# Performance work log

Hardware: AMD Instinct MI355X
Metric: run time of the kernel (lower is better)

Reference implementation:

```python
import math
import jax, jax.numpy as jnp
import numpy as np

H = 4
C_HID = 32

def setup_inputs() -> dict:
    key = jax.random.key(0)
    ks = jax.random.split(key, 8)
    B, N, C = 1, 256, 128
    q_x = jax.random.normal(ks[0], (B, N, N, C), dtype=jnp.float32)
    kv_x = jax.random.normal(ks[1], (B, N, N, C), dtype=jnp.float32)
    tri_bias = jax.random.normal(ks[2], (B, 1, H, N, N), dtype=jnp.float32)
    mask_bias = jnp.zeros((B, N, 1, 1, N), dtype=jnp.float32)
    mask = jnp.ones((B, N, N, N), dtype=jnp.float32)
    s = 1.0 / math.sqrt(C)
    Wq = jax.random.normal(ks[3], (C, H * C_HID), dtype=jnp.float32) * s
    Wk = jax.random.normal(ks[4], (C, H * C_HID), dtype=jnp.float32) * s
    Wv = jax.random.normal(ks[5], (C, H * C_HID), dtype=jnp.float32) * s
    Wg = jax.random.normal(ks[6], (C, H * C_HID), dtype=jnp.float32) * s
    Wo = jax.random.normal(ks[7], (H * C_HID, C), dtype=jnp.float32) * s
    return {"q_x": q_x, "kv_x": kv_x, "tri_bias": tri_bias, "mask_bias": mask_bias,
            "mask": mask, "Wq": Wq, "Wk": Wk, "Wv": Wv, "Wg": Wg, "Wo": Wo}

def reference(q_x, kv_x, tri_bias, mask_bias, mask, Wq, Wk, Wv, Wg, Wo):
    # q_x/kv_x: [B, N, Q, C]; mask is unused in the non-kernel path (mask_bias carries it)
    lead = q_x.shape[:-1]  # [B, N, Q]
    def split_heads(t):  # [..., H*C_HID] -> [..., H, L, C_HID]
        t = t.reshape(t.shape[:-1] + (H, C_HID))
        return jnp.swapaxes(t, -2, -3)
    q = split_heads(q_x @ Wq) / math.sqrt(C_HID)   # [B, N, H, Q, C_hid]
    k = split_heads(kv_x @ Wk)                      # [B, N, H, K, C_hid]
    v = split_heads(kv_x @ Wv)                      # [B, N, H, K, C_hid]
    a = jnp.einsum('bnhqc,bnhkc->bnhqk', q, k)
    a = a + mask_bias + tri_bias                    # biases broadcast over [B, N, H, Q, K]
    a = jax.nn.softmax(a, axis=-1)
    o = jnp.einsum('bnhqk,bnhkc->bnhqc', a, v)      # [B, N, H, Q, C_hid]
    o = jnp.swapaxes(o, -2, -3)                     # [B, N, Q, H, C_hid]
    g = jax.nn.sigmoid(q_x @ Wg).reshape(lead + (H, C_HID))
    o = o * g
    o = o.reshape(lead + (H * C_HID,))
    return o @ Wo                                   # [B, N, Q, C]
```

## Files before the change

kernel.cpp:

```cpp
#include <hip/hip_runtime.h>
#include <hip/hip_bf16.h>

#define NDIM 256
#define QDIM 256
#define CDIM 128
#define HH 4
#define DD 32
#define RROWS (NDIM * QDIM)

__device__ __forceinline__ float bf2f(unsigned short u) {
    unsigned int x = ((unsigned int)u) << 16;
    return __uint_as_float(x);
}
__device__ __forceinline__ unsigned short f2bf(float f) {
    unsigned int x = __float_as_uint(f);
    unsigned int lsb = (x >> 16) & 1u;
    x += 0x7fffu + lsb;
    return (unsigned short)(x >> 16);
}

typedef __bf16 bf16x8v __attribute__((ext_vector_type(8)));
typedef float  f32x4v  __attribute__((ext_vector_type(4)));
union frag_u { uint4 u; bf16x8v v; };

__device__ __forceinline__ bf16x8v cvt8(float4 f0, float4 f1) {
    bf16x8v r;
    r[0] = (__bf16)f0.x; r[1] = (__bf16)f0.y; r[2] = (__bf16)f0.z; r[3] = (__bf16)f0.w;
    r[4] = (__bf16)f1.x; r[5] = (__bf16)f1.y; r[6] = (__bf16)f1.z; r[7] = (__bf16)f1.w;
    return r;
}

__global__ __launch_bounds__(256, 1) void prep_weights(
    const float* __restrict__ Wq, const float* __restrict__ Wk,
    const float* __restrict__ Wv, const float* __restrict__ Wg,
    const float* __restrict__ Wo, unsigned short* __restrict__ wt)
{
    __shared__ unsigned short t[16][130];
    const int p  = blockIdx.x >> 3;
    const int ch = blockIdx.x & 7;
    const float* __restrict__ W = (p == 0) ? Wq : (p == 1) ? Wk :
                                  (p == 2) ? Wv : (p == 3) ? Wg : Wo;
    const int tid = threadIdx.x;
    for (int idx = tid; idx < 2048; idx += 256) {
        int k = idx >> 7, n = idx & 127;
        t[k][n] = f2bf(W[(ch * 16 + k) * 128 + n]);
    }
    __syncthreads();
    unsigned short* dst = wt + (size_t)p * 16384;
    for (int idx = tid; idx < 2048; idx += 256) {
        int n = idx >> 4, k = idx & 15;
        dst[n * 128 + ch * 16 + k] = t[k][n];
    }
}

__global__ __launch_bounds__(512, 4) void proj_mfma(
    const float* __restrict__ qx, const float* __restrict__ kvx,
    const unsigned short* __restrict__ wt,
    unsigned short* __restrict__ q_ws, unsigned short* __restrict__ k_ws,
    unsigned short* __restrict__ v_ws, unsigned short* __restrict__ g_ws)
{
    __shared__ unsigned short wl[2 * 16384];
    const int tid = threadIdx.x;
    const int pp = blockIdx.y;
    const float* __restrict__ X = pp ? kvx : qx;
    const unsigned short* __restrict__ WtA = wt + (size_t)(pp ? 1 : 0) * 16384;
    const unsigned short* __restrict__ WtB = wt + (size_t)(pp ? 2 : 3) * 16384;

    const int wv   = tid >> 6;
    const int lane = tid & 63;
    const int col  = lane & 15;
    const int quad = lane >> 4;
    const int r0   = blockIdx.x * 128 + wv * 16;

    const float* __restrict__ arow = X + (size_t)(r0 + col) * 128 + quad * 8;
    float4 f[4][2];
#pragma unroll
    for (int kt = 0; kt < 4; ++kt) {
        f[kt][0] = *(const float4*)(arow + kt * 32);
        f[kt][1] = *(const float4*)(arow + kt * 32 + 4);
    }

#pragma unroll
    for (int i = 0; i < 8; ++i) {
        int v = i * 512 + tid;
        int mat = v >> 11;
        int r = (v >> 4) & 127;
        int s = v & 15;
        const unsigned short* src = (mat ? WtB : WtA) + r * 128 + s * 8;
        uint4 d = *(const uint4*)src;
        *(uint4*)&wl[mat * 16384 + r * 128 + ((s ^ (r & 7)) << 3)] = d;
    }
    __syncthreads();

    frag_u a[4];
#pragma unroll
    for (int kt = 0; kt < 4; ++kt) a[kt].v = cvt8(f[kt][0], f[kt][1]);

    f32x4v accA[8], accB[8];
#pragma unroll
    for (int nt = 0; nt < 8; ++nt) {
        accA[nt] = (f32x4v){0.f, 0.f, 0.f, 0.f};
        accB[nt] = (f32x4v){0.f, 0.f, 0.f, 0.f};
    }

    const int x7 = col & 7;
#pragma unroll
    for (int kt = 0; kt < 4; ++kt) {
#pragma unroll
        for (int nt = 0; nt < 8; ++nt) {
            int off = nt * 2048 + col * 128 + ((((kt << 2) | quad) ^ x7) << 3);
            frag_u b0, b1;
            b0.u = *(const uint4*)&wl[off];
            b1.u = *(const uint4*)&wl[16384 + off];
            accA[nt] = __builtin_amdgcn_mfma_f32_16x16x32_bf16(a[kt].v, b0.v, accA[nt], 0, 0, 0);
            accB[nt] = __builtin_amdgcn_mfma_f32_16x16x32_bf16(a[kt].v, b1.v, accB[nt], 0, 0, 0);
        }
    }

#pragma unroll
    for (int r = 0; r < 4; ++r) {
        int row = r0 + quad * 4 + r;
        int n = row >> 8;
        int si = row & 255;
#pragma unroll
        for (int nt = 0; nt < 8; ++nt) {
            int c = nt * 16 + col;
            int h = c >> 5, d = c & 31;
            if (pp == 0) {
                float qv = accA[nt][r] * 0.17677669529663687f;
                q_ws[((size_t)(n * HH + h) * QDIM + si) * DD + d] = f2bf(qv);
                float s = 1.0f / (1.0f + __expf(-accB[nt][r]));
                g_ws[(size_t)row * 128 + c] = f2bf(s);
            } else {
                k_ws[((size_t)(n * HH + h) * QDIM + si) * DD + d] = f2bf(accA[nt][r]);
                v_ws[((size_t)(n * HH + h) * QDIM + si) * DD + d] = f2bf(accB[nt][r]);
            }
        }
    }
}

__global__ __launch_bounds__(256, 3) void attn_kernel(
    const unsigned short* __restrict__ q_ws, const unsigned short* __restrict__ k_ws,
    const unsigned short* __restrict__ v_ws, const unsigned short* __restrict__ g_ws,
    const float* __restrict__ tri, const float* __restrict__ mb,
    unsigned short* __restrict__ o_ws)
{
    __shared__ unsigned short vl[32 * 264];
    __shared__ unsigned short Pl[64 * 264];
    __shared__ float sinv[4][16];

    const int tid = threadIdx.x;
    const int qc = blockIdx.x;
    const int n  = blockIdx.y;
    const int h  = blockIdx.z;
    const size_t base = (size_t)(n * HH + h) * QDIM * DD;

    for (int t = 0; t < 4; ++t) {
        int idx = tid + t * 256;
        int key = idx >> 2;
        int u = idx & 3;
        union { uint4 q; unsigned short s[8]; } raw;
        raw.q = *(const uint4*)(v_ws + base + (size_t)key * DD + u * 8);
#pragma unroll
        for (int j = 0; j < 8; ++j)
            vl[(u * 8 + j) * 264 + key] = raw.s[j];
    }

    const int wv   = tid >> 6;
    const int lane = tid & 63;
    const int col  = lane & 15;
    const int quad = lane >> 4;
    const int qg   = qc * 64 + wv * 16 + col;

    frag_u bq;
    bq.u = *(const uint4*)(q_ws + base + (size_t)qg * DD + quad * 8);

    f32x4v acc[16];
#pragma unroll
    for (int mt = 0; mt < 16; ++mt) {
        int k0 = mt * 16 + quad * 4;
        float4 t4 = *(const float4*)&tri[((size_t)(h * 256 + qg)) * 256 + k0];
        float4 m4 = *(const float4*)&mb[n * 256 + k0];
        f32x4v c;
        c[0] = t4.x + m4.x; c[1] = t4.y + m4.y;
        c[2] = t4.z + m4.z; c[3] = t4.w + m4.w;
        frag_u ak;
        ak.u = *(const uint4*)(k_ws + base + (size_t)(mt * 16 + col) * DD + quad * 8);
        acc[mt] = __builtin_amdgcn_mfma_f32_16x16x32_bf16(ak.v, bq.v, c, 0, 0, 0);
    }

    float mx = -1e30f;
#pragma unroll
    for (int mt = 0; mt < 16; ++mt)
#pragma unroll
        for (int r = 0; r < 4; ++r) mx = fmaxf(mx, acc[mt][r]);
    mx = fmaxf(mx, __shfl_xor(mx, 16));
    mx = fmaxf(mx, __shfl_xor(mx, 32));

    float sum = 0.f;
#pragma unroll
    for (int mt = 0; mt < 16; ++mt)
#pragma unroll
        for (int r = 0; r < 4; ++r) {
            float e = __expf(acc[mt][r] - mx);
            acc[mt][r] = e;
            sum += e;
        }
    sum += __shfl_xor(sum, 16);
    sum += __shfl_xor(sum, 32);
    if (quad == 0) sinv[wv][col] = 1.0f / sum;

#pragma unroll
    for (int mt = 0; mt < 16; ++mt) {
        ushort4 pk;
        pk.x = f2bf(acc[mt][0]); pk.y = f2bf(acc[mt][1]);
        pk.z = f2bf(acc[mt][2]); pk.w = f2bf(acc[mt][3]);
        *(ushort4*)&Pl[(wv * 16 + col) * 264 + mt * 16 + quad * 4] = pk;
    }

    __syncthreads();

    f32x4v o0 = {0.f, 0.f, 0.f, 0.f};
    f32x4v o1 = {0.f, 0.f, 0.f, 0.f};
#pragma unroll
    for (int kc = 0; kc < 8; ++kc) {
        frag_u ap, b0, b1;
        ap.u = *(const uint4*)&Pl[(wv * 16 + col) * 264 + kc * 32 + quad * 8];
        b0.u = *(const uint4*)&vl[(col) * 264 + kc * 32 + quad * 8];
        b1.u = *(const uint4*)&vl[(16 + col) * 264 + kc * 32 + quad * 8];
        o0 = __builtin_amdgcn_mfma_f32_16x16x32_bf16(ap.v, b0.v, o0, 0, 0, 0);
        o1 = __builtin_amdgcn_mfma_f32_16x16x32_bf16(ap.v, b1.v, o1, 0, 0, 0);
    }

#pragma unroll
    for (int r = 0; r < 4; ++r) {
        int qi = quad * 4 + r;
        int qglob = qc * 64 + wv * 16 + qi;
        float iv = sinv[wv][qi];
        size_t ob = ((size_t)(n * 256 + qglob)) * 128 + h * 32;
        float g0 = bf2f(g_ws[ob + col]);
        o_ws[ob + col] = f2bf(o0[r] * iv * g0);
        float g1 = bf2f(g_ws[ob + 16 + col]);
        o_ws[ob + 16 + col] = f2bf(o1[r] * iv * g1);
    }
}

__global__ __launch_bounds__(512, 4) void outproj_mfma(
    const unsigned short* __restrict__ o_ws, const unsigned short* __restrict__ wt,
    float* __restrict__ out)
{
    __shared__ unsigned short wl[16384];
    const int tid = threadIdx.x;
    const unsigned short* __restrict__ Wt = wt + 4 * 16384;

    const int wv   = tid >> 6;
    const int lane = tid & 63;
    const int col  = lane & 15;
    const int quad = lane >> 4;
    const int r0   = blockIdx.x * 128 + wv * 16;

    frag_u a[4];
    const unsigned short* __restrict__ arow = o_ws + (size_t)(r0 + col) * 128 + quad * 8;
#pragma unroll
    for (int kt = 0; kt < 4; ++kt)
        a[kt].u = *(const uint4*)(arow + kt * 32);

#pragma unroll
    for (int i = 0; i < 4; ++i) {
        int v = i * 512 + tid;
        int r = v >> 4;
        int s = v & 15;
        uint4 d = *(const uint4*)(Wt + r * 128 + s * 8);
        *(uint4*)&wl[r * 128 + ((s ^ (r & 7)) << 3)] = d;
    }
    __syncthreads();

    f32x4v acc[8];
#pragma unroll
    for (int nt = 0; nt < 8; ++nt)
        acc[nt] = (f32x4v){0.f, 0.f, 0.f, 0.f};

    const int x7 = col & 7;
#pragma unroll
    for (int kt = 0; kt < 4; ++kt) {
#pragma unroll
        for (int nt = 0; nt < 8; ++nt) {
            int off = nt * 2048 + col * 128 + ((((kt << 2) | quad) ^ x7) << 3);
            frag_u b;
            b.u = *(const uint4*)&wl[off];
            acc[nt] = __builtin_amdgcn_mfma_f32_16x16x32_bf16(a[kt].v, b.v, acc[nt], 0, 0, 0);
        }
    }

#pragma unroll
    for (int r = 0; r < 4; ++r) {
        size_t row = r0 + quad * 4 + r;
#pragma unroll
        for (int nt = 0; nt < 8; ++nt)
            out[row * 128 + nt * 16 + col] = acc[nt][r];
    }
}

extern "C" void kernel_launch(void* const* d_in, const int* in_sizes, int n_in,
                              void* d_out, int out_size, void* d_ws, size_t ws_size,
                              hipStream_t stream) {
    const float* qx  = (const float*)d_in[0];
    const float* kvx = (const float*)d_in[1];
    const float* tri = (const float*)d_in[2];
    const float* mb  = (const float*)d_in[3];
    const float* Wq  = (const float*)d_in[5];
    const float* Wk  = (const float*)d_in[6];
    const float* Wv  = (const float*)d_in[7];
    const float* Wg  = (const float*)d_in[8];
    const float* Wo  = (const float*)d_in[9];
    float* out = (float*)d_out;

    unsigned short* ws = (unsigned short*)d_ws;
    const size_t RC = (size_t)RROWS * 128;
    unsigned short* q_ws = ws;
    unsigned short* k_ws = ws + RC;
    unsigned short* v_ws = ws + 2 * RC;
    unsigned short* g_ws = ws + 3 * RC;
    unsigned short* o_ws = ws + 4 * RC;
    unsigned short* wt   = ws + 5 * RC;

    prep_weights<<<dim3(40), 256, 0, stream>>>(Wq, Wk, Wv, Wg, Wo, wt);
    proj_mfma<<<dim3(RROWS / 128, 2), 512, 0, stream>>>(
        qx, kvx, wt, q_ws, k_ws, v_ws, g_ws);
    attn_kernel<<<dim3(4, NDIM, HH), 256, 0, stream>>>(
        q_ws, k_ws, v_ws, g_ws, tri, mb, o_ws);
    outproj_mfma<<<dim3(RROWS / 128), 512, 0, stream>>>(o_ws, wt, out);
}
```

Before: 247.9 us.

## Store V transposed and G/O head-major to drop attention LDS staging and sync

The projection kernel now writes V transposed (per head: dim-major, key-minor) and writes the gate in head-major layout. The attention kernel can then read V fragments straight from global memory, which removes the LDS transpose, the block barrier and the shared softmax-inverse array. Blocks are remapped through a 1D grid swizzle and allowed higher occupancy. The output projection reads the head-major O layout. The risk is more global/L2 traffic for V, since each wave now loads it separately, and strided transposed stores in the projection.

```diff
diff --git a/kernel.cpp b/kernel.cpp
--- a/kernel.cpp
+++ b/kernel.cpp
@@ -126,45 +126,36 @@
         for (int nt = 0; nt < 8; ++nt) {
             int c = nt * 16 + col;
             int h = c >> 5, d = c & 31;
+            size_t nh = (size_t)(n * HH + h);
             if (pp == 0) {
                 float qv = accA[nt][r] * 0.17677669529663687f;
-                q_ws[((size_t)(n * HH + h) * QDIM + si) * DD + d] = f2bf(qv);
+                q_ws[(nh * QDIM + si) * DD + d] = f2bf(qv);
                 float s = 1.0f / (1.0f + __expf(-accB[nt][r]));
-                g_ws[(size_t)row * 128 + c] = f2bf(s);
+                g_ws[(nh * QDIM + si) * DD + d] = f2bf(s);
             } else {
-                k_ws[((size_t)(n * HH + h) * QDIM + si) * DD + d] = f2bf(accA[nt][r]);
-                v_ws[((size_t)(n * HH + h) * QDIM + si) * DD + d] = f2bf(accB[nt][r]);
+                k_ws[(nh * QDIM + si) * DD + d] = f2bf(accA[nt][r]);
+                v_ws[(nh * DD + d) * QDIM + si] = f2bf(accB[nt][r]);
             }
         }
     }
 }
 
-__global__ __launch_bounds__(256, 3) void attn_kernel(
+__global__ __launch_bounds__(256, 4) void attn_kernel(
     const unsigned short* __restrict__ q_ws, const unsigned short* __restrict__ k_ws,
     const unsigned short* __restrict__ v_ws, const unsigned short* __restrict__ g_ws,
     const float* __restrict__ tri, const float* __restrict__ mb,
     unsigned short* __restrict__ o_ws)
 {
-    __shared__ unsigned short vl[32 * 264];
     __shared__ unsigned short Pl[64 * 264];
-    __shared__ float sinv[4][16];
 
     const int tid = threadIdx.x;
-    const int qc = blockIdx.x;
-    const int n  = blockIdx.y;
-    const int h  = blockIdx.z;
-    const size_t base = (size_t)(n * HH + h) * QDIM * DD;
-
-    for (int t = 0; t < 4; ++t) {
-        int idx = tid + t * 256;
-        int key = idx >> 2;
-        int u = idx & 3;
-        union { uint4 q; unsigned short s[8]; } raw;
-        raw.q = *(const uint4*)(v_ws + base + (size_t)key * DD + u * 8);
-#pragma unroll
-        for (int j = 0; j < 8; ++j)
-            vl[(u * 8 + j) * 264 + key] = raw.s[j];
-    }
+    const int b = blockIdx.x;
+    const int L = (b & 7) * 512 + (b >> 3);
+    const int qc = L & 3;
+    const int n  = (L >> 2) & 255;
+    const int h  = L >> 10;
+    const size_t base  = (size_t)(n * HH + h) * QDIM * DD;
+    const size_t vbase = (size_t)(n * HH + h) * DD * QDIM;
 
     const int wv   = tid >> 6;
     const int lane = tid & 63;
@@ -208,7 +199,7 @@
         }
     sum += __shfl_xor(sum, 16);
     sum += __shfl_xor(sum, 32);
-    if (quad == 0) sinv[wv][col] = 1.0f / sum;
+    float inv = 1.0f / sum;
 
 #pragma unroll
     for (int mt = 0; mt < 16; ++mt) {
@@ -218,16 +209,14 @@
         *(ushort4*)&Pl[(wv * 16 + col) * 264 + mt * 16 + quad * 4] = pk;
     }
 
-    __syncthreads();
-
     f32x4v o0 = {0.f, 0.f, 0.f, 0.f};
     f32x4v o1 = {0.f, 0.f, 0.f, 0.f};
 #pragma unroll
     for (int kc = 0; kc < 8; ++kc) {
         frag_u ap, b0, b1;
         ap.u = *(const uint4*)&Pl[(wv * 16 + col) * 264 + kc * 32 + quad * 8];
-        b0.u = *(const uint4*)&vl[(col) * 264 + kc * 32 + quad * 8];
-        b1.u = *(const uint4*)&vl[(16 + col) * 264 + kc * 32 + quad * 8];
+        b0.u = *(const uint4*)(v_ws + vbase + (size_t)col * QDIM + kc * 32 + quad * 8);
+        b1.u = *(const uint4*)(v_ws + vbase + (size_t)(16 + col) * QDIM + kc * 32 + quad * 8);
         o0 = __builtin_amdgcn_mfma_f32_16x16x32_bf16(ap.v, b0.v, o0, 0, 0, 0);
         o1 = __builtin_amdgcn_mfma_f32_16x16x32_bf16(ap.v, b1.v, o1, 0, 0, 0);
     }
@@ -236,8 +225,8 @@
     for (int r = 0; r < 4; ++r) {
         int qi = quad * 4 + r;
         int qglob = qc * 64 + wv * 16 + qi;
-        float iv = sinv[wv][qi];
-        size_t ob = ((size_t)(n * 256 + qglob)) * 128 + h * 32;
+        float iv = __shfl(inv, wv * 0 + qi);
+        size_t ob = (((size_t)(n * HH + h)) * QDIM + qglob) * DD;
         float g0 = bf2f(g_ws[ob + col]);
         o_ws[ob + col] = f2bf(o0[r] * iv * g0);
         float g1 = bf2f(g_ws[ob + 16 + col]);
@@ -258,12 +247,14 @@
     const int col  = lane & 15;
     const int quad = lane >> 4;
     const int r0   = blockIdx.x * 128 + wv * 16;
+    const int n    = r0 >> 8;
+    const int q0   = r0 & 255;
 
     frag_u a[4];
-    const unsigned short* __restrict__ arow = o_ws + (size_t)(r0 + col) * 128 + quad * 8;
 #pragma unroll
     for (int kt = 0; kt < 4; ++kt)
-        a[kt].u = *(const uint4*)(arow + kt * 32);
+        a[kt].u = *(const uint4*)(o_ws +
+            ((size_t)(n * HH + kt) * QDIM + q0 + col) * DD + quad * 8);
 
 #pragma unroll
     for (int i = 0; i < 4; ++i) {
@@ -327,7 +318,7 @@
     prep_weights<<<dim3(40), 256, 0, stream>>>(Wq, Wk, Wv, Wg, Wo, wt);
     proj_mfma<<<dim3(RROWS / 128, 2), 512, 0, stream>>>(
         qx, kvx, wt, q_ws, k_ws, v_ws, g_ws);
-    attn_kernel<<<dim3(4, NDIM, HH), 256, 0, stream>>>(
+    attn_kernel<<<dim3(4096), 256, 0, stream>>>(
         q_ws, k_ws, v_ws, g_ws, tri, mb, o_ws);
     outproj_mfma<<<dim3(RROWS / 128), 512, 0, stream>>>(o_ws, wt, out);
 }
```

Measured after the change: 275.9 us. 11.3% more time.
